# Kernel tuning notes

Hardware: AMD Instinct MI355X
Metric: run time of the kernel (lower is better)

## Reference

```python
import jax, jax.numpy as jnp
import numpy as np

N_NODES = 100000
N_INCID = 2000000
HIDDEN = 128
N_HE = 100000


def setup_inputs() -> dict:
    key = jax.random.key(0)
    k1, k2, k3 = jax.random.split(key, 3)
    node_feats = jax.random.normal(k1, (N_NODES, HIDDEN), dtype=jnp.float32)
    hyperedge_index = jax.random.randint(k2, (2, N_INCID), 0, N_HE, dtype=jnp.int64)
    # xavier_uniform for Linear(hidden,1): bound = sqrt(6/(hidden+1))
    bound = float(np.sqrt(6.0 / (HIDDEN + 1)))
    W = jax.random.uniform(k3, (1, HIDDEN), dtype=jnp.float32, minval=-bound, maxval=bound)
    return {"node_feats": node_feats, "hyperedge_index": hyperedge_index,
            "num_hyperedges": N_HE, "W": W}


def reference(node_feats, hyperedge_index, num_hyperedges, W):
    node_idx = hyperedge_index[0]
    he_idx = hyperedge_index[1]
    gathered = node_feats[node_idx]                      # [E, D]
    scores = jnp.einsum('ed,d->e', gathered, W[0])       # [E]
    # segment softmax over hyperedges
    seg_max = jax.ops.segment_max(scores, he_idx, num_segments=num_hyperedges)
    seg_max = jnp.where(jnp.isfinite(seg_max), seg_max, 0.0)  # empty segments
    w = jnp.exp(scores - seg_max[he_idx])                # [E]
    denom = jax.ops.segment_sum(w, he_idx, num_segments=num_hyperedges)
    w_norm = w / jnp.maximum(denom, 1e-20)[he_idx]       # [E]
    # weighted scatter-sum; empty hyperedges stay zero
    out = jax.ops.segment_sum(w_norm[:, None] * gathered, he_idx,
                              num_segments=num_hyperedges)  # [H, D]
    return out
```

## Files before the change

kernel.cpp:

```cpp
#include <hip/hip_runtime.h>
#include <hip/hip_fp16.h>
#include <math.h>

#define N_NODES 100000
#define N_INCID 2000000
#define HIDDEN  128
#define N_HE    100000

#define EPB 1024
#define FILL_BLOCKS ((N_INCID + EPB - 1) / EPB)
#define PREP_BLOCKS ((N_NODES + 3) / 4)

__device__ inline float4 h4_to_f4(uint2 p) {
    __half2 a = *(__half2*)&p.x;
    __half2 b = *(__half2*)&p.y;
    float2 fa = __half22float2(a);
    float2 fb = __half22float2(b);
    return make_float4(fa.x, fa.y, fb.x, fb.y);
}

__global__ void prep_fill_kernel(const float* __restrict__ nf,
                                 const float* __restrict__ W,
                                 const int* __restrict__ idx,
                                 float* __restrict__ en,
                                 __half2* __restrict__ nfh2,
                                 int* __restrict__ head,
                                 int2* __restrict__ next8) {
    int b = blockIdx.x;
    if (b < FILL_BLOCKS) {
        int base = b * EPB;
        int e = base + threadIdx.x;
        if (base + EPB <= N_INCID) {
            int he[4], nd[4], prev[4];
            #pragma unroll
            for (int k = 0; k < 4; ++k) {
                he[k] = idx[N_INCID + e + 256 * k];
                nd[k] = idx[e + 256 * k];
            }
            #pragma unroll
            for (int k = 0; k < 4; ++k)
                prev[k] = atomicExch(&head[he[k]], e + 256 * k);
            #pragma unroll
            for (int k = 0; k < 4; ++k)
                next8[e + 256 * k] = make_int2(nd[k], prev[k]);
        } else {
            #pragma unroll
            for (int k = 0; k < 4; ++k) {
                int ek = e + 256 * k;
                if (ek < N_INCID) {
                    int he = idx[N_INCID + ek];
                    int nd = idx[ek];
                    int prev = atomicExch(&head[he], ek);
                    next8[ek] = make_int2(nd, prev);
                }
            }
        }
    } else {
        int wave = threadIdx.x >> 6, lane = threadIdx.x & 63;
        int n = (b - FILL_BLOCKS) * 4 + wave;
        if (n >= N_NODES) return;
        const float2* nf2 = (const float2*)nf;
        const float2* w2  = (const float2*)W;
        float2 v = nf2[(size_t)n * 64 + lane];
        float2 w = w2[lane];
        float p = v.x * w.x + v.y * w.y;
        #pragma unroll
        for (int o = 32; o > 0; o >>= 1) p += __shfl_xor(p, o, 64);
        if (lane == 0) en[n] = __expf(p);
        nfh2[(size_t)n * 64 + lane] = __floats2half2_rn(v.x, v.y);
    }
}

__global__ void compute_kernel_h(const int* __restrict__ head,
                                 const int2* __restrict__ next8,
                                 const float* __restrict__ en,
                                 const uint2* __restrict__ nfh4,
                                 float* __restrict__ out) {
    int wave = threadIdx.x >> 6, lane = threadIdx.x & 63;
    int half = lane >> 5, l32 = lane & 31;
    int he = blockIdx.x * 8 + wave * 2 + half;
    if (he >= N_HE) return;

    float4 acc = make_float4(0.f, 0.f, 0.f, 0.f);
    float denom = 0.f;
    int e = head[he];
    while (e >= 0) {
        int2 p = next8[e];
        float w = en[p.x];
        float4 v = h4_to_f4(nfh4[(size_t)p.x * 32 + l32]);
        acc.x += w * v.x; acc.y += w * v.y;
        acc.z += w * v.z; acc.w += w * v.w;
        denom += w;
        e = p.y;
    }
    float inv = 1.0f / fmaxf(denom, 1e-20f);
    acc.x *= inv; acc.y *= inv; acc.z *= inv; acc.w *= inv;
    ((float4*)out)[(size_t)he * 32 + l32] = acc;
}

extern "C" void kernel_launch(void* const* d_in, const int* in_sizes, int n_in,
                              void* d_out, int out_size, void* d_ws, size_t ws_size,
                              hipStream_t stream) {
    const float* nf  = (const float*)d_in[0];
    const int*   idx = (const int*)d_in[1];
    const float* W   = (const float*)d_in[3];
    float* out = (float*)d_out;
    char* ws = (char*)d_ws;

    int*     head  = (int*)(ws + 0);
    float*   en    = (float*)(ws + 400000);
    __half2* nfh2  = (__half2*)(ws + 800000);
    int2*    next8 = (int2*)(ws + 26400000);

    hipMemsetAsync(head, 0xFF, N_HE * sizeof(int), stream);
    prep_fill_kernel<<<FILL_BLOCKS + PREP_BLOCKS, 256, 0, stream>>>(
        nf, W, idx, en, nfh2, head, next8);
    compute_kernel_h<<<(N_HE + 7) / 8, 256, 0, stream>>>(
        head, next8, en, (const uint2*)nfh2, out);
}
```

Measured before the change: 342.9 us.

## Split each hyperedge linked list into four chains for memory-level parallelism

```diff
diff --git a/kernel.cpp b/kernel.cpp
--- a/kernel.cpp
+++ b/kernel.cpp
@@ -7,9 +7,12 @@
 #define HIDDEN  128
 #define N_HE    100000
 
+#define CHAINS 4
 #define EPB 1024
 #define FILL_BLOCKS ((N_INCID + EPB - 1) / EPB)
 #define PREP_BLOCKS ((N_NODES + 3) / 4)
+
+typedef float vf4 __attribute__((ext_vector_type(4)));
 
 __device__ inline float4 h4_to_f4(uint2 p) {
     __half2 a = *(__half2*)&p.x;
@@ -38,8 +41,10 @@
                 nd[k] = idx[e + 256 * k];
             }
             #pragma unroll
-            for (int k = 0; k < 4; ++k)
-                prev[k] = atomicExch(&head[he[k]], e + 256 * k);
+            for (int k = 0; k < 4; ++k) {
+                int ek = e + 256 * k;
+                prev[k] = atomicExch(&head[(he[k] << 2) | (ek & 3)], ek);
+            }
             #pragma unroll
             for (int k = 0; k < 4; ++k)
                 next8[e + 256 * k] = make_int2(nd[k], prev[k]);
@@ -50,7 +55,7 @@
                 if (ek < N_INCID) {
                     int he = idx[N_INCID + ek];
                     int nd = idx[ek];
-                    int prev = atomicExch(&head[he], ek);
+                    int prev = atomicExch(&head[(he << 2) | (ek & 3)], ek);
                     next8[ek] = make_int2(nd, prev);
                 }
             }
@@ -81,21 +86,50 @@
     int he = blockIdx.x * 8 + wave * 2 + half;
     if (he >= N_HE) return;
 
+    const long long* __restrict__ nxt = (const long long*)next8;
+
+    int e0 = head[(he << 2) | 0];
+    int e1 = head[(he << 2) | 1];
+    int e2 = head[(he << 2) | 2];
+    int e3 = head[(he << 2) | 3];
+
     float4 acc = make_float4(0.f, 0.f, 0.f, 0.f);
     float denom = 0.f;
-    int e = head[he];
-    while (e >= 0) {
-        int2 p = next8[e];
-        float w = en[p.x];
-        float4 v = h4_to_f4(nfh4[(size_t)p.x * 32 + l32]);
-        acc.x += w * v.x; acc.y += w * v.y;
-        acc.z += w * v.z; acc.w += w * v.w;
-        denom += w;
-        e = p.y;
+
+    while ((e0 & e1 & e2 & e3) != -1) {
+        long long q0 = __builtin_nontemporal_load(&nxt[e0 < 0 ? 0 : e0]);
+        long long q1 = __builtin_nontemporal_load(&nxt[e1 < 0 ? 0 : e1]);
+        long long q2 = __builtin_nontemporal_load(&nxt[e2 < 0 ? 0 : e2]);
+        long long q3 = __builtin_nontemporal_load(&nxt[e3 < 0 ? 0 : e3]);
+
+        int n0 = (int)q0, n1 = (int)q1, n2 = (int)q2, n3 = (int)q3;
+
+        float w0 = en[n0]; w0 = (e0 >= 0) ? w0 : 0.f;
+        float w1 = en[n1]; w1 = (e1 >= 0) ? w1 : 0.f;
+        float w2 = en[n2]; w2 = (e2 >= 0) ? w2 : 0.f;
+        float w3 = en[n3]; w3 = (e3 >= 0) ? w3 : 0.f;
+
+        float4 v0 = h4_to_f4(nfh4[(size_t)n0 * 32 + l32]);
+        float4 v1 = h4_to_f4(nfh4[(size_t)n1 * 32 + l32]);
+        float4 v2 = h4_to_f4(nfh4[(size_t)n2 * 32 + l32]);
+        float4 v3 = h4_to_f4(nfh4[(size_t)n3 * 32 + l32]);
+
+        acc.x += w0 * v0.x + w1 * v1.x + w2 * v2.x + w3 * v3.x;
+        acc.y += w0 * v0.y + w1 * v1.y + w2 * v2.y + w3 * v3.y;
+        acc.z += w0 * v0.z + w1 * v1.z + w2 * v2.z + w3 * v3.z;
+        acc.w += w0 * v0.w + w1 * v1.w + w2 * v2.w + w3 * v3.w;
+        denom += (w0 + w1) + (w2 + w3);
+
+        e0 = (e0 >= 0) ? (int)(q0 >> 32) : -1;
+        e1 = (e1 >= 0) ? (int)(q1 >> 32) : -1;
+        e2 = (e2 >= 0) ? (int)(q2 >> 32) : -1;
+        e3 = (e3 >= 0) ? (int)(q3 >> 32) : -1;
     }
+
     float inv = 1.0f / fmaxf(denom, 1e-20f);
     acc.x *= inv; acc.y *= inv; acc.z *= inv; acc.w *= inv;
-    ((float4*)out)[(size_t)he * 32 + l32] = acc;
+    vf4 accv = { acc.x, acc.y, acc.z, acc.w };
+    __builtin_nontemporal_store(accv, (vf4*)&((float4*)out)[(size_t)he * 32 + l32]);
 }
 
 extern "C" void kernel_launch(void* const* d_in, const int* in_sizes, int n_in,
@@ -108,11 +142,11 @@
     char* ws = (char*)d_ws;
 
     int*     head  = (int*)(ws + 0);
-    float*   en    = (float*)(ws + 400000);
-    __half2* nfh2  = (__half2*)(ws + 800000);
-    int2*    next8 = (int2*)(ws + 26400000);
+    float*   en    = (float*)(ws + 1600000);
+    __half2* nfh2  = (__half2*)(ws + 2000000);
+    int2*    next8 = (int2*)(ws + 27600000);
 
-    hipMemsetAsync(head, 0xFF, N_HE * sizeof(int), stream);
+    hipMemsetAsync(head, 0xFF, CHAINS * N_HE * sizeof(int), stream);
     prep_fill_kernel<<<FILL_BLOCKS + PREP_BLOCKS, 256, 0, stream>>>(
         nf, W, idx, en, nfh2, head, next8);
     compute_kernel_h<<<(N_HE + 7) / 8, 256, 0, stream>>>(
```

Measured after the change: 362.0 us. +5.6%, slower.

## Split per-hyperedge linked lists into two chains to double memory-level parallelism

Applied to the files above, without the earlier changes.

```diff
diff --git a/kernel.cpp b/kernel.cpp
--- a/kernel.cpp
+++ b/kernel.cpp
@@ -7,9 +7,12 @@
 #define HIDDEN  128
 #define N_HE    100000
 
+#define CHAINS 2
 #define EPB 1024
 #define FILL_BLOCKS ((N_INCID + EPB - 1) / EPB)
 #define PREP_BLOCKS ((N_NODES + 3) / 4)
+
+typedef float vf4 __attribute__((ext_vector_type(4)));
 
 __device__ inline float4 h4_to_f4(uint2 p) {
     __half2 a = *(__half2*)&p.x;
@@ -19,56 +22,56 @@
     return make_float4(fa.x, fa.y, fb.x, fb.y);
 }
 
-__global__ void prep_fill_kernel(const float* __restrict__ nf,
-                                 const float* __restrict__ W,
-                                 const int* __restrict__ idx,
-                                 float* __restrict__ en,
-                                 __half2* __restrict__ nfh2,
-                                 int* __restrict__ head,
-                                 int2* __restrict__ next8) {
-    int b = blockIdx.x;
-    if (b < FILL_BLOCKS) {
-        int base = b * EPB;
-        int e = base + threadIdx.x;
-        if (base + EPB <= N_INCID) {
-            int he[4], nd[4], prev[4];
-            #pragma unroll
-            for (int k = 0; k < 4; ++k) {
-                he[k] = idx[N_INCID + e + 256 * k];
-                nd[k] = idx[e + 256 * k];
-            }
-            #pragma unroll
-            for (int k = 0; k < 4; ++k)
-                prev[k] = atomicExch(&head[he[k]], e + 256 * k);
-            #pragma unroll
-            for (int k = 0; k < 4; ++k)
-                next8[e + 256 * k] = make_int2(nd[k], prev[k]);
-        } else {
-            #pragma unroll
-            for (int k = 0; k < 4; ++k) {
-                int ek = e + 256 * k;
-                if (ek < N_INCID) {
-                    int he = idx[N_INCID + ek];
-                    int nd = idx[ek];
-                    int prev = atomicExch(&head[he], ek);
-                    next8[ek] = make_int2(nd, prev);
-                }
+__global__ void fill_kernel(const int* __restrict__ idx,
+                            int* __restrict__ head,
+                            int2* __restrict__ next8) {
+    int base = blockIdx.x * EPB;
+    int e = base + threadIdx.x;
+    if (base + EPB <= N_INCID) {
+        int he[4], nd[4], prev[4];
+        #pragma unroll
+        for (int k = 0; k < 4; ++k) {
+            he[k] = idx[N_INCID + e + 256 * k];
+            nd[k] = idx[e + 256 * k];
+        }
+        #pragma unroll
+        for (int k = 0; k < 4; ++k) {
+            int ek = e + 256 * k;
+            prev[k] = atomicExch(&head[(he[k] << 1) | (ek & 1)], ek);
+        }
+        #pragma unroll
+        for (int k = 0; k < 4; ++k)
+            next8[e + 256 * k] = make_int2(nd[k], prev[k]);
+    } else {
+        #pragma unroll
+        for (int k = 0; k < 4; ++k) {
+            int ek = e + 256 * k;
+            if (ek < N_INCID) {
+                int he = idx[N_INCID + ek];
+                int nd = idx[ek];
+                int prev = atomicExch(&head[(he << 1) | (ek & 1)], ek);
+                next8[ek] = make_int2(nd, prev);
             }
         }
-    } else {
-        int wave = threadIdx.x >> 6, lane = threadIdx.x & 63;
-        int n = (b - FILL_BLOCKS) * 4 + wave;
-        if (n >= N_NODES) return;
-        const float2* nf2 = (const float2*)nf;
-        const float2* w2  = (const float2*)W;
-        float2 v = nf2[(size_t)n * 64 + lane];
-        float2 w = w2[lane];
-        float p = v.x * w.x + v.y * w.y;
-        #pragma unroll
-        for (int o = 32; o > 0; o >>= 1) p += __shfl_xor(p, o, 64);
-        if (lane == 0) en[n] = __expf(p);
-        nfh2[(size_t)n * 64 + lane] = __floats2half2_rn(v.x, v.y);
     }
+}
+
+__global__ void prep_kernel(const float* __restrict__ nf,
+                            const float* __restrict__ W,
+                            float* __restrict__ en,
+                            __half2* __restrict__ nfh2) {
+    int wave = threadIdx.x >> 6, lane = threadIdx.x & 63;
+    int n = blockIdx.x * 4 + wave;
+    if (n >= N_NODES) return;
+    const float2* nf2 = (const float2*)nf;
+    const float2* w2  = (const float2*)W;
+    float2 v = nf2[(size_t)n * 64 + lane];
+    float2 w = w2[lane];
+    float p = v.x * w.x + v.y * w.y;
+    #pragma unroll
+    for (int o = 32; o > 0; o >>= 1) p += __shfl_xor(p, o, 64);
+    if (lane == 0) en[n] = __expf(p);
+    nfh2[(size_t)n * 64 + lane] = __floats2half2_rn(v.x, v.y);
 }
 
 __global__ void compute_kernel_h(const int* __restrict__ head,
@@ -81,9 +84,27 @@
     int he = blockIdx.x * 8 + wave * 2 + half;
     if (he >= N_HE) return;
 
+    int2 h2 = ((const int2*)head)[he];
+    int e0 = h2.x, e1 = h2.y;
+
     float4 acc = make_float4(0.f, 0.f, 0.f, 0.f);
     float denom = 0.f;
-    int e = head[he];
+
+    while (e0 >= 0 && e1 >= 0) {
+        int2 p0 = next8[e0];
+        int2 p1 = next8[e1];
+        float w0 = en[p0.x];
+        float w1 = en[p1.x];
+        float4 v0 = h4_to_f4(nfh4[(size_t)p0.x * 32 + l32]);
+        float4 v1 = h4_to_f4(nfh4[(size_t)p1.x * 32 + l32]);
+        acc.x += w0 * v0.x + w1 * v1.x;
+        acc.y += w0 * v0.y + w1 * v1.y;
+        acc.z += w0 * v0.z + w1 * v1.z;
+        acc.w += w0 * v0.w + w1 * v1.w;
+        denom += w0 + w1;
+        e0 = p0.y; e1 = p1.y;
+    }
+    int e = (e0 >= 0) ? e0 : e1;
     while (e >= 0) {
         int2 p = next8[e];
         float w = en[p.x];
@@ -93,9 +114,11 @@
         denom += w;
         e = p.y;
     }
+
     float inv = 1.0f / fmaxf(denom, 1e-20f);
     acc.x *= inv; acc.y *= inv; acc.z *= inv; acc.w *= inv;
-    ((float4*)out)[(size_t)he * 32 + l32] = acc;
+    vf4 accv = { acc.x, acc.y, acc.z, acc.w };
+    __builtin_nontemporal_store(accv, (vf4*)&((float4*)out)[(size_t)he * 32 + l32]);
 }
 
 extern "C" void kernel_launch(void* const* d_in, const int* in_sizes, int n_in,
@@ -108,13 +131,13 @@
     char* ws = (char*)d_ws;
 
     int*     head  = (int*)(ws + 0);
-    float*   en    = (float*)(ws + 400000);
-    __half2* nfh2  = (__half2*)(ws + 800000);
-    int2*    next8 = (int2*)(ws + 26400000);
+    float*   en    = (float*)(ws + 800000);
+    __half2* nfh2  = (__half2*)(ws + 1200000);
+    int2*    next8 = (int2*)(ws + 26800000);
 
-    hipMemsetAsync(head, 0xFF, N_HE * sizeof(int), stream);
-    prep_fill_kernel<<<FILL_BLOCKS + PREP_BLOCKS, 256, 0, stream>>>(
-        nf, W, idx, en, nfh2, head, next8);
+    hipMemsetAsync(head, 0xFF, CHAINS * N_HE * sizeof(int), stream);
+    fill_kernel<<<FILL_BLOCKS, 256, 0, stream>>>(idx, head, next8);
+    prep_kernel<<<PREP_BLOCKS, 256, 0, stream>>>(nf, W, en, nfh2);
     compute_kernel_h<<<(N_HE + 7) / 8, 256, 0, stream>>>(
         head, next8, en, (const uint2*)nfh2, out);
 }
```

New measurement: 318.1 us. 7.2% less time.

## Interleave four linked-list chains per half-wave to hide pointer-chase latency

Applied to the files above, without the earlier changes.

```diff
diff --git a/kernel.cpp b/kernel.cpp
--- a/kernel.cpp
+++ b/kernel.cpp
@@ -10,6 +10,13 @@
 #define EPB 1024
 #define FILL_BLOCKS ((N_INCID + EPB - 1) / EPB)
 #define PREP_BLOCKS ((N_NODES + 3) / 4)
+
+#define SLOTS 4
+#define HE_PER_HW 8
+#define N_HW (N_HE / HE_PER_HW)
+#define COMP_BLOCKS ((N_HW + 7) / 8)
+
+typedef float vf4 __attribute__((ext_vector_type(4)));
 
 __device__ inline float4 h4_to_f4(uint2 p) {
     __half2 a = *(__half2*)&p.x;
@@ -71,31 +78,80 @@
     }
 }
 
-__global__ void compute_kernel_h(const int* __restrict__ head,
+__global__ void compute_kernel_s(const int* __restrict__ head,
                                  const int2* __restrict__ next8,
                                  const float* __restrict__ en,
                                  const uint2* __restrict__ nfh4,
                                  float* __restrict__ out) {
     int wave = threadIdx.x >> 6, lane = threadIdx.x & 63;
     int half = lane >> 5, l32 = lane & 31;
-    int he = blockIdx.x * 8 + wave * 2 + half;
-    if (he >= N_HE) return;
+    int hw = blockIdx.x * 8 + wave * 2 + half;
+    if (hw >= N_HW) return;
+    int base = hw * HE_PER_HW;
 
-    float4 acc = make_float4(0.f, 0.f, 0.f, 0.f);
-    float denom = 0.f;
-    int e = head[he];
-    while (e >= 0) {
-        int2 p = next8[e];
-        float w = en[p.x];
-        float4 v = h4_to_f4(nfh4[(size_t)p.x * 32 + l32]);
-        acc.x += w * v.x; acc.y += w * v.y;
-        acc.z += w * v.z; acc.w += w * v.w;
-        denom += w;
-        e = p.y;
+    const long long* __restrict__ nxt = (const long long*)next8;
+
+    int heq[SLOTS], e[SLOTS];
+    float4 acc[SLOTS];
+    float den[SLOTS];
+    #pragma unroll
+    for (int s = 0; s < SLOTS; ++s) {
+        heq[s] = base + s;
+        e[s]   = head[heq[s]];
+        acc[s] = make_float4(0.f, 0.f, 0.f, 0.f);
+        den[s] = 0.f;
     }
-    float inv = 1.0f / fmaxf(denom, 1e-20f);
-    acc.x *= inv; acc.y *= inv; acc.z *= inv; acc.w *= inv;
-    ((float4*)out)[(size_t)he * 32 + l32] = acc;
+
+    while (true) {
+        if ((e[0] == -1) || (e[1] == -1) || (e[2] == -1) || (e[3] == -1)) {
+            #pragma unroll
+            for (int s = 0; s < SLOTS; ++s) {
+                while (e[s] == -1) {
+                    float inv = 1.0f / fmaxf(den[s], 1e-20f);
+                    vf4 o = { acc[s].x * inv, acc[s].y * inv,
+                              acc[s].z * inv, acc[s].w * inv };
+                    __builtin_nontemporal_store(
+                        o, (vf4*)&((float4*)out)[(size_t)heq[s] * 32 + l32]);
+                    acc[s] = make_float4(0.f, 0.f, 0.f, 0.f);
+                    den[s] = 0.f;
+                    heq[s] += SLOTS;
+                    e[s] = (heq[s] < base + HE_PER_HW) ? head[heq[s]] : -2;
+                }
+            }
+            if ((e[0] & e[1] & e[2] & e[3]) == -2) break;
+        }
+
+        long long q0 = nxt[e[0] >= 0 ? e[0] : 0];
+        long long q1 = nxt[e[1] >= 0 ? e[1] : 0];
+        long long q2 = nxt[e[2] >= 0 ? e[2] : 0];
+        long long q3 = nxt[e[3] >= 0 ? e[3] : 0];
+
+        int n0 = (int)q0, n1 = (int)q1, n2 = (int)q2, n3 = (int)q3;
+
+        float w0 = en[n0]; w0 = (e[0] >= 0) ? w0 : 0.f;
+        float w1 = en[n1]; w1 = (e[1] >= 0) ? w1 : 0.f;
+        float w2 = en[n2]; w2 = (e[2] >= 0) ? w2 : 0.f;
+        float w3 = en[n3]; w3 = (e[3] >= 0) ? w3 : 0.f;
+
+        float4 v0 = h4_to_f4(nfh4[(size_t)n0 * 32 + l32]);
+        float4 v1 = h4_to_f4(nfh4[(size_t)n1 * 32 + l32]);
+        float4 v2 = h4_to_f4(nfh4[(size_t)n2 * 32 + l32]);
+        float4 v3 = h4_to_f4(nfh4[(size_t)n3 * 32 + l32]);
+
+        acc[0].x += w0 * v0.x; acc[0].y += w0 * v0.y;
+        acc[0].z += w0 * v0.z; acc[0].w += w0 * v0.w; den[0] += w0;
+        acc[1].x += w1 * v1.x; acc[1].y += w1 * v1.y;
+        acc[1].z += w1 * v1.z; acc[1].w += w1 * v1.w; den[1] += w1;
+        acc[2].x += w2 * v2.x; acc[2].y += w2 * v2.y;
+        acc[2].z += w2 * v2.z; acc[2].w += w2 * v2.w; den[2] += w2;
+        acc[3].x += w3 * v3.x; acc[3].y += w3 * v3.y;
+        acc[3].z += w3 * v3.z; acc[3].w += w3 * v3.w; den[3] += w3;
+
+        e[0] = (e[0] >= 0) ? (int)(q0 >> 32) : -2;
+        e[1] = (e[1] >= 0) ? (int)(q1 >> 32) : -2;
+        e[2] = (e[2] >= 0) ? (int)(q2 >> 32) : -2;
+        e[3] = (e[3] >= 0) ? (int)(q3 >> 32) : -2;
+    }
 }
 
 extern "C" void kernel_launch(void* const* d_in, const int* in_sizes, int n_in,
@@ -115,6 +171,6 @@
     hipMemsetAsync(head, 0xFF, N_HE * sizeof(int), stream);
     prep_fill_kernel<<<FILL_BLOCKS + PREP_BLOCKS, 256, 0, stream>>>(
         nf, W, idx, en, nfh2, head, next8);
-    compute_kernel_h<<<(N_HE + 7) / 8, 256, 0, stream>>>(
+    compute_kernel_s<<<COMP_BLOCKS, 256, 0, stream>>>(
         head, next8, en, (const uint2*)nfh2, out);
 }
```

Result: faster. 328.7 us (-4.2%).
